# Performance work log

Hardware: AMD Instinct MI355X
Metric: run time of the kernel (lower is better)

The kernel has to match this reference:

```python
import jax, jax.numpy as jnp
import numpy as np

EPS = 1e-5


def _conv_w(x, k):
    # cross-correlation along width, kernel size 2, padding 1 -> width W+1
    xp = jnp.pad(x, ((0, 0), (0, 0), (0, 0), (1, 1)))
    return k[0] * xp[..., :-1] + k[1] * xp[..., 1:]


def _conv_h(x, k):
    # cross-correlation along height, kernel size 2, padding 1 -> height H+1
    xp = jnp.pad(x, ((0, 0), (0, 0), (1, 1), (0, 0)))
    return k[0] * xp[..., :-1, :] + k[1] * xp[..., 1:, :]


def _dwt(x, lp, hp):
    L = _conv_h(_conv_w(x, lp), lp)
    Hc = _conv_h(_conv_w(x, hp), hp)
    return L[:, :, ::2, ::2], Hc[:, :, ::2, ::2]


def _bn(y, g, b, m, v):
    # eval-mode batchnorm over channel axis 1
    scale = (g / jnp.sqrt(v + EPS))[None, :, None, None]
    shift = (b - m * g / jnp.sqrt(v + EPS))[None, :, None, None]
    return y * scale + shift


def setup_inputs() -> dict:
    key = jax.random.key(0)
    ks = jax.random.split(key, 8)
    S, B, H, W, C = 5, 8, 512, 512, 64
    x = jax.random.normal(ks[0], (B, 1, H, W), dtype=jnp.float32)
    lp = jnp.tile(jnp.array([0.7071, 0.7071], dtype=jnp.float32), (S, 1))
    hp = jnp.tile(jnp.array([0.7071, -0.7071], dtype=jnp.float32), (S, 1))
    w1 = jax.random.normal(ks[1], (S, C, 1), dtype=jnp.float32) * 0.5
    w2 = jax.random.normal(ks[2], (S, C, C), dtype=jnp.float32) * (1.0 / np.sqrt(C))
    g1 = jnp.ones((S, C), jnp.float32)
    b1 = jnp.zeros((S, C), jnp.float32)
    m1 = jax.random.normal(ks[3], (S, C), dtype=jnp.float32) * 0.1
    v1 = jax.random.uniform(ks[4], (S, C), dtype=jnp.float32) + 0.5
    g2 = jnp.ones((S, C), jnp.float32)
    b2 = jnp.zeros((S, C), jnp.float32)
    m2 = jax.random.normal(ks[5], (S, C), dtype=jnp.float32) * 0.1
    v2 = jax.random.uniform(ks[6], (S, C), dtype=jnp.float32) + 0.5
    return dict(x=x, lp=lp, hp=hp, w1=w1, w2=w2, g1=g1, b1=b1, m1=m1, v1=v1,
                g2=g2, b2=b2, m2=m2, v2=v2)


def reference(x, lp, hp, w1, w2, g1, b1, m1, v1, g2, b2, m2, v2):
    # Returns stacked-over-scale (L, H_coeff, processed_L):
    #   L, Hc: [S, B, 1, H', W'];  P: [S, B, 64, H', W']
    def per_scale(lp_s, hp_s, w1_s, g1_s, b1_s, m1_s, v1_s,
                  w2_s, g2_s, b2_s, m2_s, v2_s):
        L, Hc = _dwt(x, lp_s, hp_s)
        y = jnp.einsum('oc,bchw->bohw', w1_s, L)
        y = jax.nn.relu(_bn(y, g1_s, b1_s, m1_s, v1_s))
        y = jnp.einsum('oc,bchw->bohw', w2_s, y)
        y = jax.nn.relu(_bn(y, g2_s, b2_s, m2_s, v2_s))
        return L, Hc, y

    return jax.vmap(per_scale)(lp, hp, w1, g1, b1, m1, v1, w2, g2, b2, m2, v2)
```

## Files before the change

### kernel.cpp

```cpp
#include <hip/hip_runtime.h>
#include <math.h>

#define EPSF 1e-5f

constexpr int Sn = 5, Bn = 8, Hin = 512, Win = 512, Cn = 64;
constexpr int HO = 257, WO = 257;
constexpr int HW = HO * WO;
constexpr int NPIX = Bn * HW;
constexpr int TOTPIX = Sn * NPIX;

constexpr int WSF = 64 + Cn * 66 * 2;

typedef float f32x4 __attribute__((ext_vector_type(4)));

__global__ __launch_bounds__(64) void precompute_kernel(
    const float* __restrict__ w1, const float* __restrict__ w2,
    const float* __restrict__ g1, const float* __restrict__ b1,
    const float* __restrict__ m1, const float* __restrict__ v1,
    const float* __restrict__ g2, const float* __restrict__ b2,
    const float* __restrict__ m2, const float* __restrict__ v2,
    float* __restrict__ ws) {
    int s = blockIdx.x;
    int c = threadIdx.x;
    __shared__ float sa1[Cn], st1[Cn], stc[Cn], stS[Cn];
    __shared__ int   scS[Cn];

    int idx = s * Cn + c;
    float sc1 = g1[idx] / sqrtf(v1[idx] + EPSF);
    float a1  = sc1 * w1[idx];
    float t1  = b1[idx] - m1[idx] * sc1;
    sa1[c] = a1;
    st1[c] = t1;
    float tc = (a1 != 0.f) ? (-t1 / a1) : INFINITY;
    stc[c] = tc;
    __syncthreads();

    int rk = 0;
    for (int c2 = 0; c2 < Cn; c2++) {
        float t = stc[c2];
        rk += (t < tc) || (t == tc && c2 < c);
    }
    stS[rk] = tc;
    scS[rk] = c;
    __syncthreads();

    float* wss = ws + (size_t)s * WSF;
    wss[c] = stS[c];

    int o = c;
    float sc2 = g2[idx] / sqrtf(v2[idx] + EPSF);
    float t2o = b2[idx] - m2[idx] * sc2;
    const float* w2row = w2 + ((size_t)s * Cn + o) * Cn;

    float alpha = 0.f, beta = t2o;
    for (int cc = 0; cc < Cn; cc++) {
        float a = sa1[cc];
        bool act = (a < 0.f) || (a == 0.f && st1[cc] > 0.f);
        if (act) {
            float wf = sc2 * w2row[cc];
            alpha = fmaf(wf, a, alpha);
            beta  = fmaf(wf, st1[cc], beta);
        }
    }
    float2* abrow = (float2*)(wss + Cn);
    abrow[o * 66 + 0] = make_float2(alpha, beta);

    for (int r = 1; r <= Cn; r++) {
        int cc = scS[r - 1];
        float a = sa1[cc];
        if (a != 0.f) {
            float wf = sc2 * w2row[cc];
            float sgn = (a > 0.f) ? 1.f : -1.f;
            alpha = fmaf(sgn * wf, a, alpha);
            beta  = fmaf(sgn * wf, st1[cc], beta);
        }
        abrow[o * 66 + r] = make_float2(alpha, beta);
    }
}

constexpr int GPT = 4;
constexpr int TPB = 256;
constexpr int PIXPB = TPB * GPT;
constexpr int NCHUNK = (HW + PIXPB - 1) / PIXPB;

__device__ __forceinline__ float pwl(const float2 ab, float v) {
    return fmaxf(fmaf(ab.x, v, ab.y), 0.f);
}

__device__ __forceinline__ void dwt_lh(
    const float* __restrict__ xb, int i, int j,
    float l0, float l1, float h0, float h1,
    float& Lq, float& Hq) {
    const int r0 = 2 * i - 1, r1 = 2 * i;
    const int c0 = 2 * j - 1, c1 = 2 * j;
    const float x00 = (r0 >= 0 && r0 < Hin && c0 >= 0 ) ? xb[r0 * Win + c0] : 0.f;
    const float x01 = (r0 >= 0 && r0 < Hin && c1 < Win) ? xb[r0 * Win + c1] : 0.f;
    const float x10 = (r1 < Hin && c0 >= 0 )            ? xb[r1 * Win + c0] : 0.f;
    const float x11 = (r1 < Hin && c1 < Win)            ? xb[r1 * Win + c1] : 0.f;
    Lq = l0 * (l0 * x00 + l1 * x01) + l1 * (l0 * x10 + l1 * x11);
    Hq = h0 * (h0 * x00 + h1 * x01) + h1 * (h0 * x10 + h1 * x11);
}

__global__ __launch_bounds__(TPB) void dwt_kernel(
    const float* __restrict__ x,
    const float* __restrict__ lp, const float* __restrict__ hp,
    float* __restrict__ Lout, float* __restrict__ Hout) {
    const int tid = threadIdx.x;
    const int b = blockIdx.y, s = blockIdx.z;

    const float l0 = lp[2 * s], l1 = lp[2 * s + 1];
    const float h0 = hp[2 * s], h1 = hp[2 * s + 1];
    const float* xb = x + (size_t)b * (Hin * Win);

    const int pbase = (blockIdx.x * TPB + tid) * GPT;

    float Lv[GPT + 3];
    float Hv[GPT + 3];

    int i = pbase / WO;
    int j = pbase - i * WO;
    #pragma unroll
    for (int q = 0; q < GPT; ++q) {
        dwt_lh(xb, i, j, l0, l1, h0, h1, Lv[q], Hv[q]);
        if (++j == WO) { j = 0; ++i; }
    }
    Lv[4] = __shfl_down(Lv[0], 1, 64);  Hv[4] = __shfl_down(Hv[0], 1, 64);
    Lv[5] = __shfl_down(Lv[1], 1, 64);  Hv[5] = __shfl_down(Hv[1], 1, 64);
    Lv[6] = __shfl_down(Lv[2], 1, 64);  Hv[6] = __shfl_down(Hv[2], 1, 64);
    if ((tid & 63) == 63) {
        #pragma unroll
        for (int q = GPT; q < GPT + 3; ++q) {
            dwt_lh(xb, i, j, l0, l1, h0, h1, Lv[q], Hv[q]);
            if (++j == WO) { j = 0; ++i; }
        }
    }

    const int sb = s * Bn + b;
    const size_t lb = (size_t)sb * HW + pbase;
    const int dlt = (4 - (sb & 3)) & 3;
    const bool fast = (pbase + GPT + 3 <= HW);

    if (fast) {
        f32x4 l4, h4;
        switch (dlt) {
            case 0:  l4 = f32x4{Lv[0], Lv[1], Lv[2], Lv[3]};
                     h4 = f32x4{Hv[0], Hv[1], Hv[2], Hv[3]}; break;
            case 1:  l4 = f32x4{Lv[1], Lv[2], Lv[3], Lv[4]};
                     h4 = f32x4{Hv[1], Hv[2], Hv[3], Hv[4]}; break;
            case 2:  l4 = f32x4{Lv[2], Lv[3], Lv[4], Lv[5]};
                     h4 = f32x4{Hv[2], Hv[3], Hv[4], Hv[5]}; break;
            default: l4 = f32x4{Lv[3], Lv[4], Lv[5], Lv[6]};
                     h4 = f32x4{Hv[3], Hv[4], Hv[5], Hv[6]}; break;
        }
        *(f32x4*)(Lout + lb + dlt) = l4;
        __builtin_nontemporal_store(h4, (f32x4*)(Hout + lb + dlt));
        if (pbase == 0) {
            if (dlt > 0) { Lout[lb + 0] = Lv[0]; Hout[lb + 0] = Hv[0]; }
            if (dlt > 1) { Lout[lb + 1] = Lv[1]; Hout[lb + 1] = Hv[1]; }
            if (dlt > 2) { Lout[lb + 2] = Lv[2]; Hout[lb + 2] = Hv[2]; }
        }
    } else {
        #pragma unroll
        for (int q = 0; q < GPT; ++q) {
            if (pbase + q < HW) {
                Lout[lb + q] = Lv[q];
                Hout[lb + q] = Hv[q];
            }
        }
    }
}

__global__ __launch_bounds__(TPB) void pstore_kernel(
    const float* __restrict__ Lin,
    const float* __restrict__ ws,
    float* __restrict__ Pout) {
    __shared__ float  stS[Cn];
    __shared__ float2 sab[4 * 66];

    const int tid = threadIdx.x;
    const int og  = blockIdx.y;
    const int sb  = blockIdx.z;
    const int s   = sb >> 3;

    const float* wss = ws + (size_t)s * WSF;
    if (tid < Cn) stS[tid] = wss[tid];
    const float2* abg = (const float2*)(wss + Cn) + (size_t)og * 4 * 66;
    for (int t = tid; t < 4 * 66; t += TPB) sab[t] = abg[t];
    __syncthreads();

    const int p4 = (blockIdx.x * TPB + tid) * GPT;
    const float* Lp = Lin + (size_t)sb * HW;

    float Lv[GPT + 3];
    int   lo7[GPT + 3];

    #pragma unroll
    for (int q = 0; q < GPT; ++q) {
        const int px = p4 + q;
        const float Lq = (px < HW) ? Lp[px] : 0.f;
        Lv[q] = Lq;
        int lo = 0, hi = Cn;
        while (lo < hi) {
            const int mid = (lo + hi) >> 1;
            if (stS[mid] < Lq) lo = mid + 1; else hi = mid;
        }
        lo7[q] = lo;
    }
    Lv[4] = __shfl_down(Lv[0], 1, 64);  lo7[4] = __shfl_down(lo7[0], 1, 64);
    Lv[5] = __shfl_down(Lv[1], 1, 64);  lo7[5] = __shfl_down(lo7[1], 1, 64);
    Lv[6] = __shfl_down(Lv[2], 1, 64);  lo7[6] = __shfl_down(lo7[2], 1, 64);
    if ((tid & 63) == 63) {
        #pragma unroll
        for (int q = GPT; q < GPT + 3; ++q) {
            const int px = p4 + q;
            const float Lq = (px < HW) ? Lp[px] : 0.f;
            Lv[q] = Lq;
            int lo = 0, hi = Cn;
            while (lo < hi) {
                const int mid = (lo + hi) >> 1;
                if (stS[mid] < Lq) lo = mid + 1; else hi = mid;
            }
            lo7[q] = lo;
        }
    }

    float* const Pb = Pout + ((size_t)sb * Cn + (size_t)og * 4) * HW;

    if (p4 + GPT + 3 <= HW) {
        {
            f32x4 v = f32x4{pwl(sab[0 * 66 + lo7[0]], Lv[0]),
                            pwl(sab[0 * 66 + lo7[1]], Lv[1]),
                            pwl(sab[0 * 66 + lo7[2]], Lv[2]),
                            pwl(sab[0 * 66 + lo7[3]], Lv[3])};
            *(f32x4*)(Pb + p4) = v;
        }
        {
            f32x4 v = f32x4{pwl(sab[1 * 66 + lo7[3]], Lv[3]),
                            pwl(sab[1 * 66 + lo7[4]], Lv[4]),
                            pwl(sab[1 * 66 + lo7[5]], Lv[5]),
                            pwl(sab[1 * 66 + lo7[6]], Lv[6])};
            *(f32x4*)(Pb + (size_t)HW + p4 + 3) = v;
        }
        {
            f32x4 v = f32x4{pwl(sab[2 * 66 + lo7[2]], Lv[2]),
                            pwl(sab[2 * 66 + lo7[3]], Lv[3]),
                            pwl(sab[2 * 66 + lo7[4]], Lv[4]),
                            pwl(sab[2 * 66 + lo7[5]], Lv[5])};
            *(f32x4*)(Pb + 2 * (size_t)HW + p4 + 2) = v;
        }
        {
            f32x4 v = f32x4{pwl(sab[3 * 66 + lo7[1]], Lv[1]),
                            pwl(sab[3 * 66 + lo7[2]], Lv[2]),
                            pwl(sab[3 * 66 + lo7[3]], Lv[3]),
                            pwl(sab[3 * 66 + lo7[4]], Lv[4])};
            *(f32x4*)(Pb + 3 * (size_t)HW + p4 + 1) = v;
        }
        if (p4 == 0) {
            Pb[1 * (size_t)HW + 0] = pwl(sab[1 * 66 + lo7[0]], Lv[0]);
            Pb[1 * (size_t)HW + 1] = pwl(sab[1 * 66 + lo7[1]], Lv[1]);
            Pb[1 * (size_t)HW + 2] = pwl(sab[1 * 66 + lo7[2]], Lv[2]);
            Pb[2 * (size_t)HW + 0] = pwl(sab[2 * 66 + lo7[0]], Lv[0]);
            Pb[2 * (size_t)HW + 1] = pwl(sab[2 * 66 + lo7[1]], Lv[1]);
            Pb[3 * (size_t)HW + 0] = pwl(sab[3 * 66 + lo7[0]], Lv[0]);
        }
    } else {
        #pragma unroll
        for (int q = 0; q < GPT; ++q) {
            const int px = p4 + q;
            if (px >= HW) break;
            const float Lq = Lv[q];
            const int   r  = lo7[q];
            Pb[0 * (size_t)HW + px] = pwl(sab[0 * 66 + r], Lq);
            Pb[1 * (size_t)HW + px] = pwl(sab[1 * 66 + r], Lq);
            Pb[2 * (size_t)HW + px] = pwl(sab[2 * 66 + r], Lq);
            Pb[3 * (size_t)HW + px] = pwl(sab[3 * 66 + r], Lq);
        }
    }
}

extern "C" void kernel_launch(void* const* d_in, const int* in_sizes, int n_in,
                              void* d_out, int out_size, void* d_ws, size_t ws_size,
                              hipStream_t stream) {
    const float* x  = (const float*)d_in[0];
    const float* lp = (const float*)d_in[1];
    const float* hp = (const float*)d_in[2];
    const float* w1 = (const float*)d_in[3];
    const float* w2 = (const float*)d_in[4];
    const float* g1 = (const float*)d_in[5];
    const float* b1 = (const float*)d_in[6];
    const float* m1 = (const float*)d_in[7];
    const float* v1 = (const float*)d_in[8];
    const float* g2 = (const float*)d_in[9];
    const float* b2 = (const float*)d_in[10];
    const float* m2 = (const float*)d_in[11];
    const float* v2 = (const float*)d_in[12];

    float* out  = (float*)d_out;
    float* Lout = out;
    float* Hout = out + TOTPIX;
    float* Pout = out + 2 * TOTPIX;
    float* ws   = (float*)d_ws;

    precompute_kernel<<<Sn, Cn, 0, stream>>>(w1, w2, g1, b1, m1, v1,
                                             g2, b2, m2, v2, ws);

    dim3 grid1(NCHUNK, Bn, Sn);
    dwt_kernel<<<grid1, TPB, 0, stream>>>(x, lp, hp, Lout, Hout);

    dim3 grid2(NCHUNK, Cn / 4, Sn * Bn);
    pstore_kernel<<<grid2, TPB, 0, stream>>>(Lout, ws, Pout);
}
```

Before: 798.9 us.

## Precompute L and segment index in DWT kernel, flatten P store

```diff
diff --git a/kernel.cpp b/kernel.cpp
--- a/kernel.cpp
+++ b/kernel.cpp
@@ -8,10 +8,16 @@
 constexpr int HW = HO * WO;
 constexpr int NPIX = Bn * HW;
 constexpr int TOTPIX = Sn * NPIX;
-
-constexpr int WSF = 64 + Cn * 66 * 2;
+constexpr int NSB = Sn * Bn;
+constexpr int HWP = (HW + 3) & ~3;
+
+constexpr int    WSF    = 64 + Cn * 66 * 2;
+constexpr size_t LR_OFF = (size_t)Sn * WSF;
+constexpr unsigned PTOTu = (unsigned)((long)NSB * Cn * HW);
+constexpr size_t WS_NEED = (LR_OFF + (size_t)NSB * HWP * 2) * 4;
 
 typedef float f32x4 __attribute__((ext_vector_type(4)));
+typedef f32x4 f32x4u __attribute__((aligned(8)));
 
 __global__ __launch_bounds__(64) void precompute_kernel(
     const float* __restrict__ w1, const float* __restrict__ w2,
@@ -101,12 +107,20 @@
     Hq = h0 * (h0 * x00 + h1 * x01) + h1 * (h0 * x10 + h1 * x11);
 }
 
+template <bool WITH_LR>
 __global__ __launch_bounds__(TPB) void dwt_kernel(
     const float* __restrict__ x,
     const float* __restrict__ lp, const float* __restrict__ hp,
-    float* __restrict__ Lout, float* __restrict__ Hout) {
+    const float* __restrict__ ws_tab,
+    float* __restrict__ Lout, float* __restrict__ Hout,
+    float* __restrict__ lrws) {
+    __shared__ float stS[Cn];
     const int tid = threadIdx.x;
     const int b = blockIdx.y, s = blockIdx.z;
+    if (WITH_LR) {
+        if (tid < Cn) stS[tid] = ws_tab[(size_t)s * WSF + tid];
+        __syncthreads();
+    }
 
     const float l0 = lp[2 * s], l1 = lp[2 * s + 1];
     const float h0 = hp[2 * s], h1 = hp[2 * s + 1];
@@ -116,12 +130,21 @@
 
     float Lv[GPT + 3];
     float Hv[GPT + 3];
+    int   rr[GPT];
 
     int i = pbase / WO;
     int j = pbase - i * WO;
     #pragma unroll
     for (int q = 0; q < GPT; ++q) {
         dwt_lh(xb, i, j, l0, l1, h0, h1, Lv[q], Hv[q]);
+        if (WITH_LR) {
+            int lo = 0, hi = Cn;
+            while (lo < hi) {
+                const int mid = (lo + hi) >> 1;
+                if (stS[mid] < Lv[q]) lo = mid + 1; else hi = mid;
+            }
+            rr[q] = lo;
+        }
         if (++j == WO) { j = 0; ++i; }
     }
     Lv[4] = __shfl_down(Lv[0], 1, 64);  Hv[4] = __shfl_down(Hv[0], 1, 64);
@@ -168,9 +191,92 @@
             }
         }
     }
-}
-
-__global__ __launch_bounds__(TPB) void pstore_kernel(
+
+    if (WITH_LR) {
+        float2* lr = (float2*)lrws + (size_t)sb * HWP + pbase;
+        if (fast) {
+            f32x4 p01 = f32x4{Lv[0], (float)rr[0], Lv[1], (float)rr[1]};
+            f32x4 p23 = f32x4{Lv[2], (float)rr[2], Lv[3], (float)rr[3]};
+            *(f32x4*)(lr)     = p01;
+            *(f32x4*)(lr + 2) = p23;
+        } else {
+            #pragma unroll
+            for (int q = 0; q < GPT; ++q) {
+                if (pbase + q < HW) lr[q] = make_float2(Lv[q], (float)rr[q]);
+            }
+        }
+    }
+}
+
+constexpr int EPB = TPB * 16;
+constexpr unsigned NBLK2 = (PTOTu + EPB - 1) / EPB;
+
+__global__ __launch_bounds__(TPB) void pstore_flat(
+    const float* __restrict__ ws_tab,
+    const float* __restrict__ lrws,
+    float* __restrict__ Pout) {
+    __shared__ float2 tabs[2][66];
+
+    const int tid = threadIdx.x;
+    const unsigned base = (unsigned)blockIdx.x * (unsigned)EPB;
+    const unsigned plane_first = base / (unsigned)HW;
+    unsigned lastf = base + (unsigned)(EPB - 1);
+    if (lastf >= PTOTu) lastf = PTOTu - 1u;
+    const unsigned plane_last = lastf / (unsigned)HW;
+
+    if (tid < 132) {
+        const int slot = (tid >= 66);
+        const int idx  = slot ? tid - 66 : tid;
+        const unsigned pl = slot ? plane_last : plane_first;
+        const int s = pl >> 9;
+        const int o = pl & 63;
+        const float2* row =
+            (const float2*)(ws_tab + (size_t)s * WSF + Cn) + (size_t)o * 66;
+        tabs[slot][idx] = row[idx];
+    }
+    __syncthreads();
+
+    const float2* LR = (const float2*)lrws;
+
+    #pragma unroll
+    for (int k = 0; k < 4; ++k) {
+        const unsigned flat = base + (unsigned)k * (TPB * 4u) + (unsigned)tid * 4u;
+        if (flat >= PTOTu) break;
+        const unsigned plane = flat / (unsigned)HW;
+        const unsigned px0   = flat - plane * (unsigned)HW;
+        const int row = (plane != plane_first);
+
+        if (px0 <= (unsigned)(HW - 4) && flat + 3u < PTOTu) {
+            const float2* lr = LR + (size_t)(plane >> 6) * HWP + px0;
+            const f32x4u v01 = *(const f32x4u*)(lr);
+            const f32x4u v23 = *(const f32x4u*)(lr + 2);
+            const float2 ab0 = tabs[row][(int)v01.y];
+            const float2 ab1 = tabs[row][(int)v01.w];
+            const float2 ab2 = tabs[row][(int)v23.y];
+            const float2 ab3 = tabs[row][(int)v23.w];
+            f32x4 outv;
+            outv.x = pwl(ab0, v01.x);
+            outv.y = pwl(ab1, v01.z);
+            outv.z = pwl(ab2, v23.x);
+            outv.w = pwl(ab3, v23.z);
+            __builtin_nontemporal_store(outv, (f32x4*)(Pout + flat));
+        } else {
+            #pragma unroll
+            for (int e = 0; e < 4; ++e) {
+                const unsigned fe = flat + (unsigned)e;
+                if (fe >= PTOTu) break;
+                const unsigned pl = fe / (unsigned)HW;
+                const unsigned px = fe - pl * (unsigned)HW;
+                const int rw = (pl != plane_first);
+                const float2 lrv = LR[(size_t)(pl >> 6) * HWP + px];
+                const float2 ab  = tabs[rw][(int)lrv.y];
+                Pout[fe] = pwl(ab, lrv.x);
+            }
+        }
+    }
+}
+
+__global__ __launch_bounds__(TPB) void pstore_v5(
     const float* __restrict__ Lin,
     const float* __restrict__ ws,
     float* __restrict__ Pout) {
@@ -227,34 +333,26 @@
     float* const Pb = Pout + ((size_t)sb * Cn + (size_t)og * 4) * HW;
 
     if (p4 + GPT + 3 <= HW) {
-        {
-            f32x4 v = f32x4{pwl(sab[0 * 66 + lo7[0]], Lv[0]),
+        {   f32x4 v = f32x4{pwl(sab[0 * 66 + lo7[0]], Lv[0]),
                             pwl(sab[0 * 66 + lo7[1]], Lv[1]),
                             pwl(sab[0 * 66 + lo7[2]], Lv[2]),
                             pwl(sab[0 * 66 + lo7[3]], Lv[3])};
-            *(f32x4*)(Pb + p4) = v;
-        }
-        {
-            f32x4 v = f32x4{pwl(sab[1 * 66 + lo7[3]], Lv[3]),
+            *(f32x4*)(Pb + p4) = v; }
+        {   f32x4 v = f32x4{pwl(sab[1 * 66 + lo7[3]], Lv[3]),
                             pwl(sab[1 * 66 + lo7[4]], Lv[4]),
                             pwl(sab[1 * 66 + lo7[5]], Lv[5]),
                             pwl(sab[1 * 66 + lo7[6]], Lv[6])};
-            *(f32x4*)(Pb + (size_t)HW + p4 + 3) = v;
-        }
-        {
-            f32x4 v = f32x4{pwl(sab[2 * 66 + lo7[2]], Lv[2]),
+            *(f32x4*)(Pb + (size_t)HW + p4 + 3) = v; }
+        {   f32x4 v = f32x4{pwl(sab[2 * 66 + lo7[2]], Lv[2]),
                             pwl(sab[2 * 66 + lo7[3]], Lv[3]),
                             pwl(sab[2 * 66 + lo7[4]], Lv[4]),
                             pwl(sab[2 * 66 + lo7[5]], Lv[5])};
-            *(f32x4*)(Pb + 2 * (size_t)HW + p4 + 2) = v;
-        }
-        {
-            f32x4 v = f32x4{pwl(sab[3 * 66 + lo7[1]], Lv[1]),
+            *(f32x4*)(Pb + 2 * (size_t)HW + p4 + 2) = v; }
+        {   f32x4 v = f32x4{pwl(sab[3 * 66 + lo7[1]], Lv[1]),
                             pwl(sab[3 * 66 + lo7[2]], Lv[2]),
                             pwl(sab[3 * 66 + lo7[3]], Lv[3]),
                             pwl(sab[3 * 66 + lo7[4]], Lv[4])};
-            *(f32x4*)(Pb + 3 * (size_t)HW + p4 + 1) = v;
-        }
+            *(f32x4*)(Pb + 3 * (size_t)HW + p4 + 1) = v; }
         if (p4 == 0) {
             Pb[1 * (size_t)HW + 0] = pwl(sab[1 * 66 + lo7[0]], Lv[0]);
             Pb[1 * (size_t)HW + 1] = pwl(sab[1 * 66 + lo7[1]], Lv[1]);
@@ -305,8 +403,16 @@
                                              g2, b2, m2, v2, ws);
 
     dim3 grid1(NCHUNK, Bn, Sn);
-    dwt_kernel<<<grid1, TPB, 0, stream>>>(x, lp, hp, Lout, Hout);
-
-    dim3 grid2(NCHUNK, Cn / 4, Sn * Bn);
-    pstore_kernel<<<grid2, TPB, 0, stream>>>(Lout, ws, Pout);
-}
+
+    if (ws_size >= WS_NEED) {
+        float* lrws = ws + LR_OFF;
+        dwt_kernel<true><<<grid1, TPB, 0, stream>>>(x, lp, hp, ws,
+                                                    Lout, Hout, lrws);
+        pstore_flat<<<dim3(NBLK2), TPB, 0, stream>>>(ws, lrws, Pout);
+    } else {
+        dwt_kernel<false><<<grid1, TPB, 0, stream>>>(x, lp, hp, ws,
+                                                     Lout, Hout, nullptr);
+        dim3 grid2(NCHUNK, Cn / 4, Sn * Bn);
+        pstore_v5<<<grid2, TPB, 0, stream>>>(Lout, ws, Pout);
+    }
+}
```

After: 736.4 us. 1.08x faster.
